# Kernel optimization log

Measured on AMD Instinct MI355X. Metric: run time of the kernel, lower is better.

Reference implementation:

```python
import jax, jax.numpy as jnp
import numpy as np

B, Li, Lh, Lq, K, H, W = 256, 2, 150, 10, 40, 64, 64

def _conv(x, w, pad):
    # NCHW conv, stride 1, symmetric padding
    return jax.lax.conv_general_dilated(
        x, w, window_strides=(1, 1), padding=[(pad, pad), (pad, pad)],
        dimension_numbers=('NCHW', 'OIHW', 'NCHW'))

def setup_inputs() -> dict:
    key = jax.random.key(0)
    ks = jax.random.split(key, 8)
    g = lambda k, shape, s: jax.random.normal(k, shape, jnp.float32) * s
    return {
        'X':  g(ks[0], (B, Li, H, W), 1.0),
        'Wh': g(ks[1], (Lh, Li, 3, 3), 0.1),   # h conv weight
        'bh': jnp.zeros((Lh,), jnp.float32),     # h conv bias
        'Wr': g(ks[2], (1, Lh, 1, 1), 0.1),      # r conv (1x1, no bias)
        'Wq': g(ks[3], (Lq, 1, 3, 3), 0.1),      # q conv (no bias)
        'w':  g(ks[4], (Lq, 1, 3, 3), 0.1),      # transition weight (torch inits zeros; randomized for nontrivial grads)
        'Wc': g(ks[5], (1, H * W), 0.02),        # critic linear weight
        'bc': jnp.zeros((1,), jnp.float32),      # critic linear bias
    }

def reference(X, Wh, bh, Wr, Wq, w, Wc, bc):
    h = _conv(X, Wh, 1) + bh[None, :, None, None]   # [B,Lh,H,W]
    r = _conv(h, Wr, 0)                              # [B,1,H,W]
    q = _conv(r, Wq, 1)                              # [B,Lq,H,W]
    Wcat = jnp.concatenate([Wq, w], axis=1)          # [Lq,2,3,3]
    def step(q, _):
        v = q.max(axis=1, keepdims=True)             # [B,1,H,W]
        qn = _conv(jnp.concatenate([r, v], axis=1), Wcat, 1)
        return qn, None
    # torch: K-1 loop iterations + 1 final => K concat-convs after initial q
    q, _ = jax.lax.scan(step, q, None, length=K)
    v = q.max(axis=1, keepdims=True)
    critic = v.reshape(-1, H * W) @ Wc.T + bc        # [B,1]
    return critic, q.reshape(-1, Lq * H * W)
```

## Files before the change

### kernel.cpp

```cpp
#include <hip/hip_runtime.h>

#define HH 64
#define WW 64
#define S  68
#define PH 66
#define NLQ 10
#define NP  5
#define NR 8

typedef float f32x2 __attribute__((ext_vector_type(2)));

__global__ __launch_bounds__(512)
__attribute__((amdgpu_waves_per_eu(2, 2)))
void vin_fused(
    const float* __restrict__ X,
    const float* __restrict__ Wh,
    const float* __restrict__ bh,
    const float* __restrict__ Wr,
    const float* __restrict__ Wq,
    const float* __restrict__ wtr,
    const float* __restrict__ Wc,
    const float* __restrict__ bc,
    float* __restrict__ out)
{
  __shared__ float vb[2][PH * S];
  __shared__ float rb[PH * S];
  __shared__ float Wef[19];
  __shared__ float Wpart[152];
  __shared__ float red[8];

  const int b  = blockIdx.x;
  const int t  = threadIdx.x;
  const int x  = t & 63;
  const int yg = t >> 6;
  const int y0 = yg * NR;
  const int base0 = y0 * S + x;

  {
    float* vbf = &vb[0][0];
    for (int i = t; i < 2 * PH * S; i += 512) vbf[i] = 0.f;
    for (int i = t; i < PH * S; i += 512) rb[i] = 0.f;
  }
  __syncthreads();

  const float* Xb = X + (size_t)b * (2 * HH * WW);
  for (int i = t; i < HH * WW; i += 512) {
    const int yy = i >> 6, xx = i & 63;
    vb[0][(yy + 1) * S + xx + 1] = Xb[i];
    vb[1][(yy + 1) * S + xx + 1] = Xb[HH * WW + i];
  }
  if (t < 152) {
    const int i = t >> 3, part = t & 7;
    float s = 0.f;
    if (i < 18) {
      for (int c = part; c < 150; c += 8) s += Wr[c] * Wh[c * 18 + i];
    } else {
      for (int c = part; c < 150; c += 8) s += Wr[c] * bh[c];
    }
    Wpart[t] = s;
  }
  __syncthreads();
  if (t < 19) {
    float s = 0.f;
#pragma unroll
    for (int k = 0; k < 8; ++k) s += Wpart[t * 8 + k];
    Wef[t] = s;
  }
  __syncthreads();

  {
    float We[19];
#pragma unroll
    for (int i = 0; i < 19; ++i) We[i] = Wef[i];
#pragma unroll
    for (int j = 0; j < NR; ++j) {
      const int tb = base0 + j * S;
      float s = We[18];
#pragma unroll
      for (int dy = 0; dy < 3; ++dy)
#pragma unroll
        for (int dx = 0; dx < 3; ++dx) {
          const int idx = tb + dy * S + dx;
          s = fmaf(vb[0][idx], We[dy * 3 + dx], s);
          s = fmaf(vb[1][idx], We[9 + dy * 3 + dx], s);
        }
      rb[tb + S + 1] = s;
    }
  }
  __syncthreads();

  f32x2 q0p[NR][NP];
  {
    float win[NR + 2][3];
#pragma unroll
    for (int rr = 0; rr < NR + 2; ++rr) {
      const int a = base0 + rr * S;
      win[rr][0] = rb[a];
      win[rr][1] = rb[a + 1];
      win[rr][2] = rb[a + 2];
    }
    f32x2 mm[NR];
#pragma unroll
    for (int p = 0; p < NP; ++p) {
      f32x2 w[9];
#pragma unroll
      for (int k = 0; k < 9; ++k)
        w[k] = (f32x2){ Wq[(2 * p) * 9 + k], Wq[(2 * p + 1) * 9 + k] };
#pragma unroll
      for (int j = 0; j < NR; ++j) {
        f32x2 acc = (f32x2){0.f, 0.f};
#pragma unroll
        for (int dy = 0; dy < 3; ++dy)
#pragma unroll
          for (int dx = 0; dx < 3; ++dx) {
            const float wv = win[j + dy][dx];
            acc = __builtin_elementwise_fma(w[dy * 3 + dx], (f32x2){wv, wv}, acc);
          }
        q0p[j][p] = acc;
        mm[j] = (p == 0) ? acc : __builtin_elementwise_max(mm[j], acc);
      }
    }
#pragma unroll
    for (int j = 0; j < NR; ++j)
      vb[0][base0 + (j + 1) * S + 1] = fmaxf(mm[j].x, mm[j].y);
  }
  __syncthreads();

  f32x2 wtp[NP][9];
#pragma unroll
  for (int p = 0; p < NP; ++p)
#pragma unroll
    for (int k = 0; k < 9; ++k)
      wtp[p][k] = (f32x2){ wtr[(2 * p) * 9 + k], wtr[(2 * p + 1) * 9 + k] };

  auto step = [&](const float* __restrict__ vin, float* __restrict__ vout) {
    float win[NR + 2][3];
#pragma unroll
    for (int rr = 0; rr < NR + 2; ++rr) {
      const int a = base0 + rr * S;
      win[rr][0] = vin[a];
      win[rr][1] = vin[a + 1];
      win[rr][2] = vin[a + 2];
    }
    f32x2 mm[NR];
#pragma unroll
    for (int p = 0; p < NP; ++p) {
      f32x2 w[9];
#pragma unroll
      for (int k = 0; k < 9; ++k) w[k] = wtp[p][k];
#pragma unroll
      for (int j = 0; j < NR; ++j) {
        f32x2 acc = q0p[j][p];
#pragma unroll
        for (int dy = 0; dy < 3; ++dy)
#pragma unroll
          for (int dx = 0; dx < 3; ++dx) {
            const float wv = win[j + dy][dx];
            acc = __builtin_elementwise_fma(w[dy * 3 + dx], (f32x2){wv, wv}, acc);
          }
        mm[j] = (p == 0) ? acc : __builtin_elementwise_max(mm[j], acc);
      }
    }
#pragma unroll
    for (int j = 0; j < NR; ++j)
      vout[base0 + (j + 1) * S + 1] = fmaxf(mm[j].x, mm[j].y);
    __syncthreads();
  };

#pragma unroll 1
  for (int s2 = 0; s2 < 19; ++s2) { step(vb[0], vb[1]); step(vb[1], vb[0]); }
  step(vb[0], vb[1]);

  float wcv[NR];
#pragma unroll
  for (int j = 0; j < NR; ++j) wcv[j] = Wc[(y0 + j) * WW + x];

  float* qo = out + 256 + (size_t)b * (NLQ * HH * WW) + y0 * WW + x;
  float acc_c = 0.f;
  {
    const float* vin = vb[1];
    float win[NR + 2][3];
#pragma unroll
    for (int rr = 0; rr < NR + 2; ++rr) {
      const int a = base0 + rr * S;
      win[rr][0] = vin[a];
      win[rr][1] = vin[a + 1];
      win[rr][2] = vin[a + 2];
    }
    f32x2 mm[NR];
#pragma unroll
    for (int p = 0; p < NP; ++p) {
      f32x2 w[9];
#pragma unroll
      for (int k = 0; k < 9; ++k) w[k] = wtp[p][k];
#pragma unroll
      for (int j = 0; j < NR; ++j) {
        f32x2 acc = q0p[j][p];
#pragma unroll
        for (int dy = 0; dy < 3; ++dy)
#pragma unroll
          for (int dx = 0; dx < 3; ++dx) {
            const float wv = win[j + dy][dx];
            acc = __builtin_elementwise_fma(w[dy * 3 + dx], (f32x2){wv, wv}, acc);
          }
        qo[(2 * p)     * (HH * WW) + j * WW] = acc.x;
        qo[(2 * p + 1) * (HH * WW) + j * WW] = acc.y;
        mm[j] = (p == 0) ? acc : __builtin_elementwise_max(mm[j], acc);
      }
    }
#pragma unroll
    for (int j = 0; j < NR; ++j)
      acc_c = fmaf(fmaxf(mm[j].x, mm[j].y), wcv[j], acc_c);
  }

#pragma unroll
  for (int off = 32; off > 0; off >>= 1) acc_c += __shfl_down(acc_c, off);
  if (x == 0) red[yg] = acc_c;
  __syncthreads();
  if (t == 0) {
    float s = bc[0];
#pragma unroll
    for (int i = 0; i < 8; ++i) s += red[i];
    out[b] = s;
  }
}

extern "C" void kernel_launch(void* const* d_in, const int* in_sizes, int n_in,
                              void* d_out, int out_size, void* d_ws, size_t ws_size,
                              hipStream_t stream) {
  (void)n_in; (void)out_size; (void)d_ws; (void)ws_size;
  const float* X   = (const float*)d_in[0];
  const float* Wh  = (const float*)d_in[1];
  const float* bh  = (const float*)d_in[2];
  const float* Wr  = (const float*)d_in[3];
  const float* Wq  = (const float*)d_in[4];
  const float* wtr = (const float*)d_in[5];
  const float* Wc  = (const float*)d_in[6];
  const float* bc  = (const float*)d_in[7];
  float* out = (float*)d_out;

  const int B = in_sizes[0] / (2 * HH * WW);
  vin_fused<<<B, 512, 0, stream>>>(X, Wh, bh, Wr, Wq, wtr, Wc, bc, out);
}
```

Before: 162.8 us.

## Replace per-step block barriers with neighbor-wave LDS flag synchronization

Turns the 39 value-iteration steps into a single loop in which each wave (one 8-row band) only waits for its two adjacent bands. Before waiting, it computes the six interior rows, which need no halo data. It then spins on volatile shared-memory flags before loading the halo rows and computing the two edge rows, and publishes its progress through a flag. This removes the full-block __syncthreads per step and lets waves drift and overlap, at the cost of spin-wait loops on LDS and reliance on the double-buffer ordering being correct with at most one step of skew.

```diff
diff --git a/kernel.cpp b/kernel.cpp
--- a/kernel.cpp
+++ b/kernel.cpp
@@ -28,6 +28,7 @@
   __shared__ float Wef[19];
   __shared__ float Wpart[152];
   __shared__ float red[8];
+  __shared__ int   flg[8];
 
   const int b  = blockIdx.x;
   const int t  = threadIdx.x;
@@ -36,10 +37,13 @@
   const int y0 = yg * NR;
   const int base0 = y0 * S + x;
 
+  volatile int* vflg = flg;
+
   {
     float* vbf = &vb[0][0];
     for (int i = t; i < 2 * PH * S; i += 512) vbf[i] = 0.f;
     for (int i = t; i < PH * S; i += 512) rb[i] = 0.f;
+    if (t < 8) flg[t] = -1;
   }
   __syncthreads();
 
@@ -133,15 +137,20 @@
     for (int k = 0; k < 9; ++k)
       wtp[p][k] = (f32x2){ wtr[(2 * p) * 9 + k], wtr[(2 * p + 1) * 9 + k] };
 
-  auto step = [&](const float* __restrict__ vin, float* __restrict__ vout) {
+#pragma unroll 1
+  for (int it = 0; it < 39; ++it) {
+    const float* vin  = vb[it & 1];
+    float*       vout = vb[(it + 1) & 1];
+
     float win[NR + 2][3];
 #pragma unroll
-    for (int rr = 0; rr < NR + 2; ++rr) {
+    for (int rr = 1; rr <= 8; ++rr) {
       const int a = base0 + rr * S;
       win[rr][0] = vin[a];
       win[rr][1] = vin[a + 1];
       win[rr][2] = vin[a + 2];
     }
+
     f32x2 mm[NR];
 #pragma unroll
     for (int p = 0; p < NP; ++p) {
@@ -149,7 +158,7 @@
 #pragma unroll
       for (int k = 0; k < 9; ++k) w[k] = wtp[p][k];
 #pragma unroll
-      for (int j = 0; j < NR; ++j) {
+      for (int j = 1; j <= 6; ++j) {
         f32x2 acc = q0p[j][p];
 #pragma unroll
         for (int dy = 0; dy < 3; ++dy)
@@ -161,15 +170,53 @@
         mm[j] = (p == 0) ? acc : __builtin_elementwise_max(mm[j], acc);
       }
     }
+
+    if (yg > 0) { while (vflg[yg - 1] < it - 1) {} }
+    if (yg < 7) { while (vflg[yg + 1] < it - 1) {} }
+    __threadfence_block();
+
+    {
+      const int a0 = base0;
+      win[0][0] = vin[a0];
+      win[0][1] = vin[a0 + 1];
+      win[0][2] = vin[a0 + 2];
+      const int a9 = base0 + 9 * S;
+      win[9][0] = vin[a9];
+      win[9][1] = vin[a9 + 1];
+      win[9][2] = vin[a9 + 2];
+    }
+
+#pragma unroll
+    for (int p = 0; p < NP; ++p) {
+      f32x2 w[9];
+#pragma unroll
+      for (int k = 0; k < 9; ++k) w[k] = wtp[p][k];
+      f32x2 acc0 = q0p[0][p];
+      f32x2 acc7 = q0p[7][p];
+#pragma unroll
+      for (int dy = 0; dy < 3; ++dy)
+#pragma unroll
+        for (int dx = 0; dx < 3; ++dx) {
+          const int k = dy * 3 + dx;
+          const float w0 = win[dy][dx];
+          acc0 = __builtin_elementwise_fma(w[k], (f32x2){w0, w0}, acc0);
+          const float w7 = win[7 + dy][dx];
+          acc7 = __builtin_elementwise_fma(w[k], (f32x2){w7, w7}, acc7);
+        }
+      mm[0] = (p == 0) ? acc0 : __builtin_elementwise_max(mm[0], acc0);
+      mm[7] = (p == 0) ? acc7 : __builtin_elementwise_max(mm[7], acc7);
+    }
+
 #pragma unroll
     for (int j = 0; j < NR; ++j)
       vout[base0 + (j + 1) * S + 1] = fmaxf(mm[j].x, mm[j].y);
-    __syncthreads();
-  };
-
-#pragma unroll 1
-  for (int s2 = 0; s2 < 19; ++s2) { step(vb[0], vb[1]); step(vb[1], vb[0]); }
-  step(vb[0], vb[1]);
+    __threadfence_block();
+    if (x == 0) vflg[yg] = it;
+  }
+
+  if (yg > 0) { while (vflg[yg - 1] < 38) {} }
+  if (yg < 7) { while (vflg[yg + 1] < 38) {} }
+  __threadfence_block();
 
   float wcv[NR];
 #pragma unroll
```

After: 172.6 us. 1.06x slower.

## Keep value map in registers and exchange halos via bpermute and small LDS

Applied to the files above, without the earlier changes.

The recurrent value map now stays in each thread's registers across the 40 iterations instead of being written to and re-read from a padded LDS buffer. Vertical halo rows go through a small double-buffered LDS array, and horizontal neighbours come from ds_bpermute lane exchanges. This removes the 30 LDS reads and 8 writes per thread per step, in exchange for two barriers per iteration instead of one and 20 bpermutes per step.

```diff
diff --git a/kernel.cpp b/kernel.cpp
--- a/kernel.cpp
+++ b/kernel.cpp
@@ -25,6 +25,7 @@
 {
   __shared__ float vb[2][PH * S];
   __shared__ float rb[PH * S];
+  __shared__ float hv[2][16][64];
   __shared__ float Wef[19];
   __shared__ float Wpart[152];
   __shared__ float red[8];
@@ -35,6 +36,9 @@
   const int yg = t >> 6;
   const int y0 = yg * NR;
   const int base0 = y0 * S + x;
+
+  const int idxL = ((x - 1) & 63) << 2;
+  const int idxR = ((x + 1) & 63) << 2;
 
   {
     float* vbf = &vb[0][0];
@@ -90,6 +94,7 @@
   __syncthreads();
 
   f32x2 q0p[NR][NP];
+  float vv[10];
   {
     float win[NR + 2][3];
 #pragma unroll
@@ -121,10 +126,8 @@
       }
     }
 #pragma unroll
-    for (int j = 0; j < NR; ++j)
-      vb[0][base0 + (j + 1) * S + 1] = fmaxf(mm[j].x, mm[j].y);
-  }
-  __syncthreads();
+    for (int j = 0; j < NR; ++j) vv[j + 1] = fmaxf(mm[j].x, mm[j].y);
+  }
 
   f32x2 wtp[NP][9];
 #pragma unroll
@@ -133,15 +136,29 @@
     for (int k = 0; k < 9; ++k)
       wtp[p][k] = (f32x2){ wtr[(2 * p) * 9 + k], wtr[(2 * p + 1) * 9 + k] };
 
-  auto step = [&](const float* __restrict__ vin, float* __restrict__ vout) {
-    float win[NR + 2][3];
-#pragma unroll
-    for (int rr = 0; rr < NR + 2; ++rr) {
-      const int a = base0 + rr * S;
-      win[rr][0] = vin[a];
-      win[rr][1] = vin[a + 1];
-      win[rr][2] = vin[a + 2];
-    }
+  __syncthreads();
+
+#pragma unroll 1
+  for (int it = 0; it < 39; ++it) {
+    const int pb = it & 1;
+    hv[pb][yg * 2][x]     = vv[1];
+    hv[pb][yg * 2 + 1][x] = vv[8];
+    __syncthreads();
+    vv[0] = (yg > 0) ? hv[pb][yg * 2 - 1][x] : 0.f;
+    vv[9] = (yg < 7) ? hv[pb][yg * 2 + 2][x] : 0.f;
+    __syncthreads();
+
+    float vL[10], vR[10];
+#pragma unroll
+    for (int r = 0; r < 10; ++r) {
+      const float bl = __int_as_float(
+          __builtin_amdgcn_ds_bpermute(idxL, __float_as_int(vv[r])));
+      const float br = __int_as_float(
+          __builtin_amdgcn_ds_bpermute(idxR, __float_as_int(vv[r])));
+      vL[r] = (x == 0)  ? 0.f : bl;
+      vR[r] = (x == 63) ? 0.f : br;
+    }
+
     f32x2 mm[NR];
 #pragma unroll
     for (int p = 0; p < NP; ++p) {
@@ -151,42 +168,47 @@
 #pragma unroll
       for (int j = 0; j < NR; ++j) {
         f32x2 acc = q0p[j][p];
-#pragma unroll
-        for (int dy = 0; dy < 3; ++dy)
-#pragma unroll
-          for (int dx = 0; dx < 3; ++dx) {
-            const float wv = win[j + dy][dx];
-            acc = __builtin_elementwise_fma(w[dy * 3 + dx], (f32x2){wv, wv}, acc);
-          }
+        acc = __builtin_elementwise_fma(w[0], (f32x2){vL[j],     vL[j]},     acc);
+        acc = __builtin_elementwise_fma(w[1], (f32x2){vv[j],     vv[j]},     acc);
+        acc = __builtin_elementwise_fma(w[2], (f32x2){vR[j],     vR[j]},     acc);
+        acc = __builtin_elementwise_fma(w[3], (f32x2){vL[j + 1], vL[j + 1]}, acc);
+        acc = __builtin_elementwise_fma(w[4], (f32x2){vv[j + 1], vv[j + 1]}, acc);
+        acc = __builtin_elementwise_fma(w[5], (f32x2){vR[j + 1], vR[j + 1]}, acc);
+        acc = __builtin_elementwise_fma(w[6], (f32x2){vL[j + 2], vL[j + 2]}, acc);
+        acc = __builtin_elementwise_fma(w[7], (f32x2){vv[j + 2], vv[j + 2]}, acc);
+        acc = __builtin_elementwise_fma(w[8], (f32x2){vR[j + 2], vR[j + 2]}, acc);
         mm[j] = (p == 0) ? acc : __builtin_elementwise_max(mm[j], acc);
       }
     }
 #pragma unroll
-    for (int j = 0; j < NR; ++j)
-      vout[base0 + (j + 1) * S + 1] = fmaxf(mm[j].x, mm[j].y);
-    __syncthreads();
-  };
-
-#pragma unroll 1
-  for (int s2 = 0; s2 < 19; ++s2) { step(vb[0], vb[1]); step(vb[1], vb[0]); }
-  step(vb[0], vb[1]);
-
-  float wcv[NR];
-#pragma unroll
-  for (int j = 0; j < NR; ++j) wcv[j] = Wc[(y0 + j) * WW + x];
-
-  float* qo = out + 256 + (size_t)b * (NLQ * HH * WW) + y0 * WW + x;
-  float acc_c = 0.f;
-  {
-    const float* vin = vb[1];
-    float win[NR + 2][3];
-#pragma unroll
-    for (int rr = 0; rr < NR + 2; ++rr) {
-      const int a = base0 + rr * S;
-      win[rr][0] = vin[a];
-      win[rr][1] = vin[a + 1];
-      win[rr][2] = vin[a + 2];
-    }
+    for (int j = 0; j < NR; ++j) vv[j + 1] = fmaxf(mm[j].x, mm[j].y);
+  }
+
+  {
+    const int pb = 39 & 1;
+    hv[pb][yg * 2][x]     = vv[1];
+    hv[pb][yg * 2 + 1][x] = vv[8];
+    __syncthreads();
+    vv[0] = (yg > 0) ? hv[pb][yg * 2 - 1][x] : 0.f;
+    vv[9] = (yg < 7) ? hv[pb][yg * 2 + 2][x] : 0.f;
+    __syncthreads();
+
+    float vL[10], vR[10];
+#pragma unroll
+    for (int r = 0; r < 10; ++r) {
+      const float bl = __int_as_float(
+          __builtin_amdgcn_ds_bpermute(idxL, __float_as_int(vv[r])));
+      const float br = __int_as_float(
+          __builtin_amdgcn_ds_bpermute(idxR, __float_as_int(vv[r])));
+      vL[r] = (x == 0)  ? 0.f : bl;
+      vR[r] = (x == 63) ? 0.f : br;
+    }
+
+    float wcv[NR];
+#pragma unroll
+    for (int j = 0; j < NR; ++j) wcv[j] = Wc[(y0 + j) * WW + x];
+
+    float* qo = out + 256 + (size_t)b * (NLQ * HH * WW) + y0 * WW + x;
     f32x2 mm[NR];
 #pragma unroll
     for (int p = 0; p < NP; ++p) {
@@ -196,32 +218,35 @@
 #pragma unroll
       for (int j = 0; j < NR; ++j) {
         f32x2 acc = q0p[j][p];
-#pragma unroll
-        for (int dy = 0; dy < 3; ++dy)
-#pragma unroll
-          for (int dx = 0; dx < 3; ++dx) {
-            const float wv = win[j + dy][dx];
-            acc = __builtin_elementwise_fma(w[dy * 3 + dx], (f32x2){wv, wv}, acc);
-          }
+        acc = __builtin_elementwise_fma(w[0], (f32x2){vL[j],     vL[j]},     acc);
+        acc = __builtin_elementwise_fma(w[1], (f32x2){vv[j],     vv[j]},     acc);
+        acc = __builtin_elementwise_fma(w[2], (f32x2){vR[j],     vR[j]},     acc);
+        acc = __builtin_elementwise_fma(w[3], (f32x2){vL[j + 1], vL[j + 1]}, acc);
+        acc = __builtin_elementwise_fma(w[4], (f32x2){vv[j + 1], vv[j + 1]}, acc);
+        acc = __builtin_elementwise_fma(w[5], (f32x2){vR[j + 1], vR[j + 1]}, acc);
+        acc = __builtin_elementwise_fma(w[6], (f32x2){vL[j + 2], vL[j + 2]}, acc);
+        acc = __builtin_elementwise_fma(w[7], (f32x2){vv[j + 2], vv[j + 2]}, acc);
+        acc = __builtin_elementwise_fma(w[8], (f32x2){vR[j + 2], vR[j + 2]}, acc);
         qo[(2 * p)     * (HH * WW) + j * WW] = acc.x;
         qo[(2 * p + 1) * (HH * WW) + j * WW] = acc.y;
         mm[j] = (p == 0) ? acc : __builtin_elementwise_max(mm[j], acc);
       }
     }
+    float acc_c = 0.f;
 #pragma unroll
     for (int j = 0; j < NR; ++j)
       acc_c = fmaf(fmaxf(mm[j].x, mm[j].y), wcv[j], acc_c);
-  }
-
-#pragma unroll
-  for (int off = 32; off > 0; off >>= 1) acc_c += __shfl_down(acc_c, off);
-  if (x == 0) red[yg] = acc_c;
-  __syncthreads();
-  if (t == 0) {
-    float s = bc[0];
-#pragma unroll
-    for (int i = 0; i < 8; ++i) s += red[i];
-    out[b] = s;
+
+#pragma unroll
+    for (int off = 32; off > 0; off >>= 1) acc_c += __shfl_down(acc_c, off);
+    if (x == 0) red[yg] = acc_c;
+    __syncthreads();
+    if (t == 0) {
+      float s = bc[0];
+#pragma unroll
+      for (int i = 0; i < 8; ++i) s += red[i];
+      out[b] = s;
+    }
   }
 }
 
```

New measurement: 185.2 us. 13.7% more time.
